# Optimization experiments

Hardware: AMD Instinct MI355X
Metric: run time of the kernel (lower is better)

Reference implementation:

```python
import jax, jax.numpy as jnp
import numpy as np

B, T, N, F = 4, 24, 10000, 64
E = 160000
K_STEPS = 3
HID = 128


def setup_inputs() -> dict:
    key = jax.random.key(0)
    ks = jax.random.split(key, 12)
    history = jax.random.normal(ks[0], (B, T, N, F), dtype=jnp.float32)
    horizon = jax.random.normal(ks[1], (B, 6, N, F), dtype=jnp.float32)
    edge_index = jax.random.randint(ks[2], (2, E), 0, N, dtype=jnp.int64)
    s = 1.0 / np.sqrt(F)
    W_enc = jax.random.normal(ks[3], (F, F), dtype=jnp.float32) * s
    W_hor = jax.random.normal(ks[4], (F, F), dtype=jnp.float32) * s
    b_enc = jnp.zeros((F,), dtype=jnp.float32)
    W_fc = jax.random.normal(ks[5], (F, F), dtype=jnp.float32) * s  # EventGAN.fc (no bias)
    b_gcn = jax.random.normal(ks[6], (F,), dtype=jnp.float32) * 0.01  # EventGAN.bias
    W1 = jax.random.normal(ks[7], (T * F, HID), dtype=jnp.float32) / np.sqrt(T * F)
    b1 = jnp.zeros((HID,), dtype=jnp.float32)
    W2 = jax.random.normal(ks[8], (HID, 1), dtype=jnp.float32) / np.sqrt(HID)
    b2 = jnp.zeros((1,), dtype=jnp.float32)
    return {"history": history, "horizon": horizon, "edge_index": edge_index,
            "W_enc": W_enc, "W_hor": W_hor, "b_enc": b_enc,
            "W_fc": W_fc, "b_gcn": b_gcn,
            "W1": W1, "b1": b1, "W2": W2, "b2": b2}


def _event_gan_step(h, row, col, norm, W_fc, b_gcn, n_nodes):
    # h: [B, N, F]; GCN-style normalized sum aggregation (EventGAN.forward)
    x = h @ W_fc  # fc, no bias
    msgs = norm[None, :, None] * x[:, row, :]  # [B, Etot, F] gather + scale
    agg = jax.vmap(lambda m: jax.ops.segment_sum(m, col, num_segments=n_nodes))(msgs)
    return agg + b_gcn


def reference(history, horizon, edge_index, W_enc, W_hor, b_enc, W_fc, b_gcn, W1, b1, W2, b2):
    b, t, n, f = history.shape
    # FeatureEncoder (stand-in): per-timestep linear over F mixing pooled horizon context
    hor_ctx = jnp.mean(horizon, axis=1) @ W_hor  # [B, N, F]
    x = jnp.tanh(jnp.einsum('btnf,fg->btng', history, W_enc) + hor_ctx[:, None, :, :] + b_enc)
    # spatial: k-step EventGAN propagation on last timestep's exogenous features
    h = x[:, -1, :, -f:]  # [B, N, F] (F == exogenous_features)
    row0, col0 = edge_index[0], edge_index[1]
    loops = jnp.arange(n, dtype=edge_index.dtype)
    row = jnp.concatenate([row0, loops])
    col = jnp.concatenate([col0, loops])
    deg = jax.ops.segment_sum(jnp.ones_like(col, dtype=h.dtype), col, num_segments=n)
    dinv = jnp.where(deg > 0, jax.lax.rsqrt(jnp.maximum(deg, 1.0)), 0.0)
    norm = dinv[row] * dinv[col]
    for _ in range(K_STEPS):
        h = _event_gan_step(h, row, col, norm, W_fc, b_gcn, n)
    x = x.at[:, -1, :, -f:].set(h)
    # temporal MLP (stand-in): flatten per-node time series -> scalar
    flat = x.transpose(0, 2, 1, 3).reshape(b * n, t * f)
    out = jax.nn.relu(flat @ W1 + b1) @ W2 + b2  # [B*N, 1]
    return out.reshape(b, n)
```

## Files before the change

kernel.cpp:

```cpp
#include <hip/hip_runtime.h>

constexpr int cB = 4, cT = 24, cN = 10000, cF = 64, cE = 160000, cHID = 128, cK = 3;

typedef short s16x4 __attribute__((ext_vector_type(4)));
typedef short s16x8 __attribute__((ext_vector_type(8)));
typedef float f32x16 __attribute__((ext_vector_type(16)));

__device__ __forceinline__ unsigned short f2bf(float f) {
    union { float f; unsigned u; } c; c.f = f;
    unsigned u = c.u;
    return (unsigned short)((u + 0x7FFFu + ((u >> 16) & 1u)) >> 16);
}
__device__ __forceinline__ unsigned short f2bf_rtz(float f) {
    union { float f; unsigned u; } c; c.f = f;
    return (unsigned short)(c.u >> 16);
}
__device__ __forceinline__ unsigned asu(float f) {
    union { float f; unsigned u; } c; c.f = f; return c.u;
}

__device__ __forceinline__ float tanh_fast(float x) {
    float e = __expf(2.0f * x);
    return 1.0f - 2.0f * __builtin_amdgcn_rcpf(e + 1.0f);
}

__global__ void k_zeroA(int* __restrict__ cnt_in, int* __restrict__ cursor) {
    int i = blockIdx.x * 256 + threadIdx.x;
    if (i < cN) { cnt_in[i] = 0; cursor[i] = 0; }
}

__global__ void k_count(const int* __restrict__ edges, int* __restrict__ cnt_in) {
    int e = blockIdx.x * 256 + threadIdx.x;
    int nz = __syncthreads_count(e < cE && edges[2 * e + 1] == 0);
    if (e < cE) {
        int m = (nz == 256) ? 2 : 1;
        atomicAdd(&cnt_in[edges[m * (cE + e)]], 1);
    }
}

__global__ void k_scan(const int* __restrict__ cnt_in, int* __restrict__ rowptr,
                       float* __restrict__ dinv) {
    int lane = threadIdx.x;
    int carry = 0;
    for (int base = 0; base < cN; base += 1024) {
        int i0 = base + lane * 16;
        int v[16];
        int sum16 = 0;
        #pragma unroll
        for (int k = 0; k < 16; k++) {
            v[k] = (i0 + k < cN) ? cnt_in[i0 + k] : 0;
            sum16 += v[k];
        }
        int s = sum16;
        #pragma unroll
        for (int d = 1; d < 64; d <<= 1) {
            int u = __shfl_up(s, d, 64);
            if (lane >= d) s += u;
        }
        int pre = carry + s - sum16;
        #pragma unroll
        for (int k = 0; k < 16; k++) {
            if (i0 + k < cN) {
                rowptr[i0 + k] = pre;
                dinv[i0 + k] = rsqrtf((float)(v[k] + 1));
            }
            pre += v[k];
        }
        carry += __shfl(s, 63, 64);
    }
    if (lane == 0) rowptr[cN] = carry;
}

__global__ void k_fill(const int* __restrict__ edges, const int* __restrict__ rowptr,
                       int* __restrict__ cursor, int* __restrict__ csr_src) {
    int e = blockIdx.x * 256 + threadIdx.x;
    int nz = __syncthreads_count(e < cE && edges[2 * e + 1] == 0);
    if (e < cE) {
        int m = (nz == 256) ? 2 : 1;
        int r = edges[m * e];
        int c = edges[m * (cE + e)];
        int pos = atomicAdd(&cursor[c], 1);
        csr_src[rowptr[c] + pos] = r;
    }
}

__launch_bounds__(256)
__global__ void k_prep(const float* __restrict__ horizon, const float* __restrict__ W_hor,
                       const float* __restrict__ b_enc, float* __restrict__ hc,
                       const float* __restrict__ W1, unsigned short* __restrict__ W1T,
                       int hcB) {
    __shared__ float sLDS[64 * 65];
    __shared__ float sm[4][64];
    const int tid = threadIdx.x;
    if ((int)blockIdx.x < hcB) {
        float* sW = sLDS;
        {
            const float4* src = (const float4*)W_hor;
            float4* dst = (float4*)sW;
            #pragma unroll
            for (int q = 0; q < 4; q++) dst[tid + q * 256] = src[tid + q * 256];
        }
        int g = tid & 63;
        int sub = tid >> 6;
        int pair = blockIdx.x * 4 + sub;
        bool ok = pair < cB * cN;
        float m = 0.f;
        if (ok) {
            int b = pair / cN, n = pair % cN;
            const float* hp = horizon + ((size_t)(b * 6) * cN + n) * 64 + g;
            #pragma unroll
            for (int hh = 0; hh < 6; hh++) m += hp[(size_t)hh * cN * 64];
            m *= (1.0f / 6.0f);
        }
        sm[sub][g] = m;
        __syncthreads();
        if (!ok) return;
        float a = b_enc[g];
        #pragma unroll 8
        for (int f = 0; f < 64; f++) a = fmaf(sm[sub][f], sW[f * 64 + g], a);
        hc[(size_t)pair * 64 + g] = a;
    } else {
        float (*sT)[65] = (float(*)[65])sLDS;
        const int wb = blockIdx.x - hcB;
        const int t = wb % cT;
        const int hx = (wb / cT) * 64;
        const int gx = t * 64;
        #pragma unroll
        for (int r = 0; r < 4; r++) {
            int flat = tid + r * 256;
            int gp = flat >> 4, h4 = (flat & 15) * 4;
            float4 v = *(const float4*)&W1[(size_t)(gx + gp) * cHID + hx + h4];
            sT[h4 + 0][gp] = v.x; sT[h4 + 1][gp] = v.y;
            sT[h4 + 2][gp] = v.z; sT[h4 + 3][gp] = v.w;
        }
        __syncthreads();
        #pragma unroll
        for (int r = 0; r < 2; r++) {
            int flat = tid + r * 256;
            int h = flat >> 3, seg = flat & 7;
            s16x8 o;
            #pragma unroll
            for (int i = 0; i < 8; i++) o[i] = (short)f2bf(sT[h][seg * 8 + i]);
            *(s16x8*)&W1T[((size_t)t * cHID + hx + h) * 64 + seg * 8] = o;
        }
    }
}

__launch_bounds__(128, 2)
__global__ void k_encode_mlp(const float* __restrict__ history,
                             const float* __restrict__ W_enc,
                             const float* __restrict__ hc,
                             const unsigned short* __restrict__ W1T,
                             const float* __restrict__ dinv,
                             float* __restrict__ accbuf,
                             float* __restrict__ y0) {
    __shared__ unsigned short sHist[2][32 * 64];
    __shared__ unsigned short sXe[32 * 64];
    const int tid = threadIdx.x;
    const int lane = tid & 63;
    const int w = tid >> 6;
    const int l31 = lane & 31;
    const int lhi = lane >> 5;
    const int n0 = blockIdx.x * 32;
    const int b = blockIdx.y;
    const int zz = blockIdx.z;
    const int t0 = zz * (cT / 2), t1 = t0 + (cT / 2);
    const int nn = min(32, cN - n0);
    const int col = w * 32 + l31;

    float4 r[4];
    auto RLOAD = [&](int t) {
        const float* hsrc = history + ((size_t)(b * cT + t) * cN + n0) * 64;
        #pragma unroll
        for (int q = 0; q < 4; q++) {
            int flat = tid + q * 128;
            int node = flat >> 4, fq = flat & 15;
            r[q] = make_float4(0.f, 0.f, 0.f, 0.f);
            if (node < nn) r[q] = *(const float4*)(hsrc + node * 64 + fq * 4);
        }
    };
    auto SSTORE = [&](int buf) {
        #pragma unroll
        for (int q = 0; q < 4; q++) {
            int flat = tid + q * 128;
            int node = flat >> 4, fq = flat & 15;
            int2 p;
            p.x = (int)__builtin_amdgcn_perm(asu(r[q].y), asu(r[q].x), 0x07060302u);
            p.y = (int)__builtin_amdgcn_perm(asu(r[q].w), asu(r[q].z), 0x07060302u);
            int idx = (node * 64 + fq * 4) ^ ((node & 7) << 3);
            *(int2*)&sHist[buf][idx] = p;
        }
    };

    s16x8 wenc[4];
    #pragma unroll
    for (int ks = 0; ks < 4; ks++)
        #pragma unroll
        for (int i = 0; i < 8; i++)
            wenc[ks][i] = (short)f2bf(W_enc[(ks * 16 + lhi * 8 + i) * 64 + col]);

    float hcr[16];
    float dvr[16];
    #pragma unroll
    for (int reg = 0; reg < 16; reg++) {
        int row = (reg & 3) + 8 * (reg >> 2) + 4 * lhi;
        bool okr = row < nn;
        hcr[reg] = okr ? hc[(size_t)(b * cN + n0 + row) * 64 + col] : 0.f;
        dvr[reg] = okr ? dinv[n0 + row] : 0.f;
    }

    f32x16 accm[2];
    #pragma unroll
    for (int ht = 0; ht < 2; ht++)
        #pragma unroll
        for (int rr = 0; rr < 16; rr++) accm[ht][rr] = 0.f;

    RLOAD(t0);
    SSTORE(0);
    int cur = 0;

    for (int t = t0; t < t1; t++) {
        const bool last = (t == cT - 1);
        const bool have_next = (t + 1 < t1);
        if (have_next) RLOAD(t + 1);
        __syncthreads();
        f32x16 d;
        #pragma unroll
        for (int reg = 0; reg < 16; reg++) d[reg] = hcr[reg];
        {
            int base = l31 * 64 + lhi * 8;
            int sw = (l31 & 7) << 3;
            #pragma unroll
            for (int ks = 0; ks < 4; ks++) {
                s16x8 a = *(const s16x8*)&sHist[cur][(base + ks * 16) ^ sw];
                d = __builtin_amdgcn_mfma_f32_32x32x16_bf16(a, wenc[ks], d, 0, 0, 0);
            }
        }
        if (last) {
            #pragma unroll
            for (int reg = 0; reg < 16; reg++) {
                int row = (reg & 3) + 8 * (reg >> 2) + 4 * lhi;
                if (row < nn)
                    y0[(size_t)(n0 + row) * (cB * 64) + b * 64 + col] =
                        dvr[reg] * tanh_fast(d[reg]);
            }
        } else {
            #pragma unroll
            for (int reg = 0; reg < 16; reg++) {
                int row = (reg & 3) + 8 * (reg >> 2) + 4 * lhi;
                int idx = (row * 64 + col) ^ ((row & 7) << 3);
                sXe[idx] = f2bf_rtz(tanh_fast(d[reg]));
            }
            __syncthreads();
            int bbase = l31 * 64 + lhi * 8;
            int swB = (l31 & 7) << 3;
            #pragma unroll
            for (int ht = 0; ht < 2; ht++) {
                const unsigned short* wrow =
                    W1T + ((size_t)t * cHID + (w * 64 + ht * 32 + l31)) * 64 + lhi * 8;
                #pragma unroll
                for (int ks = 0; ks < 4; ks++) {
                    s16x8 aw = *(const s16x8*)(wrow + ks * 16);
                    s16x8 bx = *(const s16x8*)&sXe[(bbase + ks * 16) ^ swB];
                    accm[ht] = __builtin_amdgcn_mfma_f32_32x32x16_bf16(aw, bx, accm[ht], 0, 0, 0);
                }
            }
        }
        if (have_next) SSTORE(cur ^ 1);
        cur ^= 1;
    }
    int node = l31;
    if (node < nn) {
        float* ap = accbuf + (size_t)zz * cB * cN * cHID + (size_t)(b * cN + n0 + node) * cHID;
        #pragma unroll
        for (int ht = 0; ht < 2; ht++) {
            #pragma unroll
            for (int q = 0; q < 4; q++) {
                int hid0 = w * 64 + ht * 32 + q * 8 + lhi * 4;
                float4 v = make_float4(accm[ht][q * 4 + 0], accm[ht][q * 4 + 1],
                                       accm[ht][q * 4 + 2], accm[ht][q * 4 + 3]);
                *(float4*)(ap + hid0) = v;
            }
        }
    }
}

__launch_bounds__(512)
__global__ void k_gstep(const int* __restrict__ rowptr, const int* __restrict__ csr_src,
                        const float* __restrict__ dinv, const float* __restrict__ yin,
                        const float* __restrict__ W_fc, const float* __restrict__ b_gcn,
                        float* __restrict__ yout, int lastStep) {
    __shared__ float sW[64 * 64];
    __shared__ float sAgg[4][4][64];
    const int tid = threadIdx.x;
    {
        const float4* src = (const float4*)W_fc;
        float4* dst = (float4*)sW;
        #pragma unroll
        for (int q = 0; q < 2; q++) dst[tid + q * 512] = src[tid + q * 512];
    }
    const int wv = tid >> 6;
    const int nl = wv >> 1;
    const int bp = wv & 1;
    const int g = tid & 63;
    const int n = blockIdx.x * 4 + nl;
    if (n < cN) {
        const float* yn = yin + (size_t)n * 256 + bp * 128;
        float a0 = yn[g], a1 = yn[64 + g];
        int i = rowptr[n], end = rowptr[n + 1];
        for (; i + 4 <= end; i += 4) {
            int s0 = csr_src[i + 0], s1 = csr_src[i + 1];
            int s2 = csr_src[i + 2], s3 = csr_src[i + 3];
            const float* x0 = yin + (size_t)s0 * 256 + bp * 128;
            const float* x1 = yin + (size_t)s1 * 256 + bp * 128;
            const float* x2 = yin + (size_t)s2 * 256 + bp * 128;
            const float* x3 = yin + (size_t)s3 * 256 + bp * 128;
            float v00 = x0[g], v01 = x0[64 + g];
            float v10 = x1[g], v11 = x1[64 + g];
            float v20 = x2[g], v21 = x2[64 + g];
            float v30 = x3[g], v31 = x3[64 + g];
            a0 += (v00 + v10) + (v20 + v30);
            a1 += (v01 + v11) + (v21 + v31);
        }
        for (; i < end; i++) {
            int s = csr_src[i];
            const float* xs = yin + (size_t)s * 256 + bp * 128;
            a0 += xs[g]; a1 += xs[64 + g];
        }
        sAgg[nl][bp * 2 + 0][g] = a0;
        sAgg[nl][bp * 2 + 1][g] = a1;
    }
    __syncthreads();
    if (n >= cN) return;
    const float* g0 = sAgg[nl][bp * 2 + 0];
    const float* g1 = sAgg[nl][bp * 2 + 1];
    float o0 = 0.f, o1 = 0.f;
    #pragma unroll 8
    for (int f = 0; f < 64; f++) {
        float wv_ = sW[f * 64 + g];
        o0 = fmaf(g0[f], wv_, o0);
        o1 = fmaf(g1[f], wv_, o1);
    }
    float di = dinv[n], bg = b_gcn[g];
    float h0v = fmaf(di, o0, bg);
    float h1v = fmaf(di, o1, bg);
    if (!lastStep) { h0v *= di; h1v *= di; }
    yout[(size_t)n * 256 + (bp * 2 + 0) * 64 + g] = h0v;
    yout[(size_t)n * 256 + (bp * 2 + 1) * 64 + g] = h1v;
}

__launch_bounds__(128)
__global__ void k_head(const float* __restrict__ accbuf, const float* __restrict__ hfin,
                       const float* __restrict__ W1, const float* __restrict__ b1,
                       const float* __restrict__ W2, const float* __restrict__ b2,
                       float* __restrict__ out) {
    __shared__ float sW1[64 * cHID];
    __shared__ float sh[64];
    __shared__ float red[2];
    const int tid = threadIdx.x;
    {
        const float4* src = (const float4*)(W1 + (size_t)(cT - 1) * 64 * cHID);
        float4* dst = (float4*)sW1;
        #pragma unroll
        for (int q = 0; q < 16; q++) dst[tid + q * 128] = src[tid + q * 128];
    }
    float w2j = W2[tid];
    float b1j = b1[tid];
    int pbase = blockIdx.x * 16;
    for (int p = 0; p < 16; p++) {
        int pair = pbase + p;
        if (pair >= cB * cN) break;
        int b = pair / cN, n = pair % cN;
        __syncthreads();
        if (tid < 64) sh[tid] = hfin[(size_t)n * 256 + b * 64 + tid];
        __syncthreads();
        float a = accbuf[(size_t)pair * cHID + tid]
                + accbuf[(size_t)cB * cN * cHID + (size_t)pair * cHID + tid] + b1j;
        #pragma unroll 8
        for (int f = 0; f < 64; f++) a = fmaf(sh[f], sW1[f * cHID + tid], a);
        a = fmaxf(a, 0.f) * w2j;
        #pragma unroll
        for (int d = 32; d > 0; d >>= 1) a += __shfl_down(a, d, 64);
        if ((tid & 63) == 0) red[tid >> 6] = a;
        __syncthreads();
        if (tid == 0) out[pair] = red[0] + red[1] + b2[0];
    }
}

extern "C" void kernel_launch(void* const* d_in, const int* in_sizes, int n_in,
                              void* d_out, int out_size, void* d_ws, size_t ws_size,
                              hipStream_t stream) {
    const float* history = (const float*)d_in[0];
    const float* horizon = (const float*)d_in[1];
    const int*   edges   = (const int*)d_in[2];
    const float* W_enc   = (const float*)d_in[3];
    const float* W_hor   = (const float*)d_in[4];
    const float* b_enc   = (const float*)d_in[5];
    const float* W_fc    = (const float*)d_in[6];
    const float* b_gcn   = (const float*)d_in[7];
    const float* W1      = (const float*)d_in[8];
    const float* b1      = (const float*)d_in[9];
    const float* W2      = (const float*)d_in[10];
    const float* b2      = (const float*)d_in[11];
    float* out = (float*)d_out;

    float* ws = (float*)d_ws;
    float* hc     = ws;
    float* accbuf = hc + (size_t)cB * cN * 64;
    float* yA     = accbuf + (size_t)2 * cB * cN * cHID;
    float* yB     = yA + (size_t)cB * cN * 64;
    float* dinv   = yB + (size_t)cB * cN * 64;
    unsigned short* w1t = (unsigned short*)(dinv + cN);
    int*   cnt_in = (int*)(w1t + (size_t)cT * cHID * 64);
    int*   cursor = cnt_in + cN;
    int*   rowptr = cursor + cN;
    int*   csr_src= rowptr + cN + 1;

    const int hcB = (cB * cN + 3) / 4;

    k_zeroA<<<(cN + 255) / 256, 256, 0, stream>>>(cnt_in, cursor);
    k_count<<<(cE + 255) / 256, 256, 0, stream>>>(edges, cnt_in);
    k_scan<<<1, 64, 0, stream>>>(cnt_in, rowptr, dinv);
    k_fill<<<(cE + 255) / 256, 256, 0, stream>>>(edges, rowptr, cursor, csr_src);

    k_prep<<<hcB + cT * 2, 256, 0, stream>>>(horizon, W_hor, b_enc, hc, W1, w1t, hcB);
    k_encode_mlp<<<dim3((cN + 31) / 32, cB, 2), 128, 0, stream>>>(history, W_enc, hc,
                                                                  w1t, dinv, accbuf, yA);

    k_gstep<<<(cN + 3) / 4, 512, 0, stream>>>(rowptr, csr_src, dinv, yA, W_fc, b_gcn, yB, 0);
    k_gstep<<<(cN + 3) / 4, 512, 0, stream>>>(rowptr, csr_src, dinv, yB, W_fc, b_gcn, yA, 0);
    k_gstep<<<(cN + 3) / 4, 512, 0, stream>>>(rowptr, csr_src, dinv, yA, W_fc, b_gcn, yB, 1);

    k_head<<<(cB * cN + 15) / 16, 128, 0, stream>>>(accbuf, yB, W1, b1, W2, b2, out);
}
```

Measured before the change: 362.1 us.

## Stream history tiles into LDS via global_load_lds DMA instead of register staging

Replaces the register-staged prefetch (global load into registers, bf16 pack, LDS store) with direct global-to-LDS loads of fp32 history into an XOR-swizzled double buffer. The bf16 conversion moves to the consumer side after the LDS read. The aim is to cut VGPR pressure and the store instructions on the critical path so the copy overlaps with the MFMA work. In exchange LDS use doubles (fp32 instead of bf16) and each wave does more LDS read traffic. Synchronization relies on a single __syncthreads with no explicit vmcnt wait for the async loads, which could be a correctness hazard.

```diff
diff --git a/kernel.cpp b/kernel.cpp
--- a/kernel.cpp
+++ b/kernel.cpp
@@ -154,7 +154,7 @@
                              const float* __restrict__ dinv,
                              float* __restrict__ accbuf,
                              float* __restrict__ y0) {
-    __shared__ unsigned short sHist[2][32 * 64];
+    __shared__ float sHistF[2][32 * 64];
     __shared__ unsigned short sXe[32 * 64];
     const int tid = threadIdx.x;
     const int lane = tid & 63;
@@ -168,27 +168,15 @@
     const int nn = min(32, cN - n0);
     const int col = w * 32 + l31;
 
-    float4 r[4];
-    auto RLOAD = [&](int t) {
+    auto DMA = [&](int t, int buf) {
         const float* hsrc = history + ((size_t)(b * cT + t) * cN + n0) * 64;
         #pragma unroll
-        for (int q = 0; q < 4; q++) {
-            int flat = tid + q * 128;
-            int node = flat >> 4, fq = flat & 15;
-            r[q] = make_float4(0.f, 0.f, 0.f, 0.f);
-            if (node < nn) r[q] = *(const float4*)(hsrc + node * 64 + fq * 4);
-        }
-    };
-    auto SSTORE = [&](int buf) {
-        #pragma unroll
-        for (int q = 0; q < 4; q++) {
-            int flat = tid + q * 128;
-            int node = flat >> 4, fq = flat & 15;
-            int2 p;
-            p.x = (int)__builtin_amdgcn_perm(asu(r[q].y), asu(r[q].x), 0x07060302u);
-            p.y = (int)__builtin_amdgcn_perm(asu(r[q].w), asu(r[q].z), 0x07060302u);
-            int idx = (node * 64 + fq * 4) ^ ((node & 7) << 3);
-            *(int2*)&sHist[buf][idx] = p;
+        for (int k = 0; k < 4; k++) {
+            int unit = (w * 4 + k) * 64 + lane;
+            int node = unit >> 4, us = unit & 15;
+            int u = us ^ (node & 7);
+            const float* g = (node < nn) ? (hsrc + node * 64 + u * 4) : hsrc;
+            __builtin_amdgcn_global_load_lds(g, &sHistF[buf][(w * 4 + k) * 256], 16, 0, 0);
         }
     };
 
@@ -215,25 +203,31 @@
         #pragma unroll
         for (int rr = 0; rr < 16; rr++) accm[ht][rr] = 0.f;
 
-    RLOAD(t0);
-    SSTORE(0);
+    DMA(t0, 0);
     int cur = 0;
 
     for (int t = t0; t < t1; t++) {
         const bool last = (t == cT - 1);
         const bool have_next = (t + 1 < t1);
-        if (have_next) RLOAD(t + 1);
-        __syncthreads();
+        __syncthreads();
+        if (have_next) DMA(t + 1, cur ^ 1);
         f32x16 d;
         #pragma unroll
         for (int reg = 0; reg < 16; reg++) d[reg] = hcr[reg];
         {
-            int base = l31 * 64 + lhi * 8;
-            int sw = (l31 & 7) << 3;
+            const float* rowp = &sHistF[cur][l31 * 64];
+            const int mm = l31 & 7;
             #pragma unroll
             for (int ks = 0; ks < 4; ks++) {
-                s16x8 a = *(const s16x8*)&sHist[cur][(base + ks * 16) ^ sw];
-                d = __builtin_amdgcn_mfma_f32_32x32x16_bf16(a, wenc[ks], d, 0, 0, 0);
+                int u0 = ks * 4 + lhi * 2;
+                float4 v0 = *(const float4*)&rowp[((u0 + 0) ^ mm) * 4];
+                float4 v1 = *(const float4*)&rowp[((u0 + 1) ^ mm) * 4];
+                union { s16x8 s; unsigned u[4]; } a;
+                a.u[0] = __builtin_amdgcn_perm(asu(v0.y), asu(v0.x), 0x07060302u);
+                a.u[1] = __builtin_amdgcn_perm(asu(v0.w), asu(v0.z), 0x07060302u);
+                a.u[2] = __builtin_amdgcn_perm(asu(v1.y), asu(v1.x), 0x07060302u);
+                a.u[3] = __builtin_amdgcn_perm(asu(v1.w), asu(v1.z), 0x07060302u);
+                d = __builtin_amdgcn_mfma_f32_32x32x16_bf16(a.s, wenc[ks], d, 0, 0, 0);
             }
         }
         if (last) {
@@ -266,7 +260,6 @@
                 }
             }
         }
-        if (have_next) SSTORE(cur ^ 1);
         cur ^= 1;
     }
     int node = l31;
```

Measured after the change: 370.5 us. 1.02x slower.
